# Kernel optimization log

Measured on AMD Instinct MI355X. Metric: run time of the kernel, lower is better.

The kernel has to match this reference:

```python
import jax, jax.numpy as jnp
import numpy as np


def setup_inputs() -> dict:
    key = jax.random.key(0)
    ks = jax.random.split(key, 11)
    B, Cin, H, W = 4, 3, 256, 256
    width, m1, m2, L = 64, 16, 16, 4
    def n(k, shape, scale=1.0):
        return (scale * jax.random.normal(k, shape)).astype(jnp.float32)
    spec_scale = 1.0 / (width * width)  # matches torch scale = 1/(in_ch*out_ch)
    return {
        "x": n(ks[0], (B, Cin, H, W)),
        "fc0_w": n(ks[1], (width, Cin), 0.1),
        "fc0_b": n(ks[2], (width,), 0.1),
        "spec_wr": n(ks[3], (L, width, width, m1, m2), spec_scale),
        "spec_wi": n(ks[4], (L, width, width, m1, m2), spec_scale),
        "w_w": n(ks[5], (L, width, width), 0.1),
        "w_b": n(ks[6], (L, width), 0.1),
        "fc1_w": n(ks[7], (128, width), 0.1),
        "fc1_b": n(ks[8], (128,), 0.1),
        "fc2_w": n(ks[9], (1, 128), 0.1),
        "fc2_b": n(ks[10], (1,), 0.1),
    }


def conv1x1(x, w, b):
    # x: (B,C,H,W), w: (O,C), b: (O,) -- equivalent to nn.Conv2d(C,O,1)
    return jnp.einsum('bchw,oc->bohw', x, w) + b[None, :, None, None]


def spectral_conv2d(x, wr, wi):
    # x: (B,C,H,W); wr/wi: (C,O,m1,m2) real/imag parts of cfloat weight
    B, C, H, W = x.shape
    m1, m2 = wr.shape[2], wr.shape[3]
    O = wr.shape[1]
    x_ft = jnp.fft.rfft2(x)                       # (B,C,H,W//2+1) complex64
    w = wr + 1j * wi
    blk = jnp.einsum('bixy,ioxy->boxy', x_ft[:, :, :m1, :m2], w)
    out_ft = jnp.zeros((B, O, H, W // 2 + 1), dtype=blk.dtype)
    out_ft = out_ft.at[:, :, :m1, :m2].set(blk)
    return jnp.fft.irfft2(out_ft, s=(H, W))


def reference(x, fc0_w, fc0_b, spec_wr, spec_wi, w_w, w_b, fc1_w, fc1_b, fc2_w, fc2_b):
    h = conv1x1(x, fc0_w, fc0_b)
    n_layers = spec_wr.shape[0]
    for i in range(n_layers):
        h = spectral_conv2d(h, spec_wr[i], spec_wi[i]) + conv1x1(h, w_w[i], w_b[i])
        h = jax.nn.gelu(h, approximate=False)
    h = jax.nn.gelu(conv1x1(h, fc1_w, fc1_b), approximate=False)
    return conv1x1(h, fc2_w, fc2_b)
```

## Files before the change

kernel.cpp:

```cpp
#include <hip/hip_runtime.h>
#include <math.h>

#define HW 65536

typedef __attribute__((ext_vector_type(8))) short short8;
typedef __attribute__((ext_vector_type(4))) float f32x4;

__device__ __forceinline__ unsigned bf16rne(float f) {
  union { float f; unsigned u; } a; a.f = f;
  return (a.u + 0x7fffu + ((a.u >> 16) & 1u)) >> 16;
}
__device__ __forceinline__ float bf16tof(unsigned h) {
  union { unsigned u; float f; } a; a.u = h << 16;
  return a.f;
}
__device__ __forceinline__ float gelu(float v) {
  float ax = fabsf(v) * 0.70710678118654752f;
  float t = 1.0f / fmaf(0.3275911f, ax, 1.0f);
  float p = t * (0.254829592f +
           t * (-0.284496736f +
           t * (1.421413741f +
           t * (-1.453152027f +
           t * 1.061405429f))));
  float e = __expf(-ax * ax);
  float er = copysignf(fmaf(-p, e, 1.0f), v);
  return 0.5f * v * (1.0f + er);
}

__global__ __launch_bounds__(256) void k_tables(float* __restrict__ cosT, float* __restrict__ sinT,
                                                ushort* __restrict__ eah, ushort* __restrict__ eal,
                                                ushort* __restrict__ e2h, ushort* __restrict__ e2l,
                                                const float* __restrict__ ww, const float* __restrict__ w1,
                                                ushort* __restrict__ wh, ushort* __restrict__ wl,
                                                ushort* __restrict__ w1h, ushort* __restrict__ w1l) {
  int idx = blockIdx.x * 256 + threadIdx.x;
  const float w = 0.0245436926061702596f;
  if (idx < 4096) {
    int k = idx >> 8, xx = idx & 255;
    int t = (k * xx) & 255;
    float ang = (float)t * w;
    cosT[idx] = cosf(ang);
    sinT[idx] = sinf(ang);
  } else if (idx < 12288) {
    int e = idx - 4096;
    int j = e >> 8, xx = e & 255;
    int k = j >> 1;
    int t = (k * xx) & 255;
    float ang = (float)t * w;
    float val = (j & 1) ? -sinf(ang) : cosf(ang);
    unsigned hi = bf16rne(val);
    unsigned lo = bf16rne(val - bf16tof(hi));
    eah[j * 256 + xx] = (ushort)hi;
    eal[j * 256 + xx] = (ushort)lo;
    e2h[xx * 32 + j] = (ushort)hi;
    e2l[xx * 32 + j] = (ushort)lo;
  } else if (idx < 28672) {
    int j = idx - 12288;
    float v = ww[j];
    unsigned hi = bf16rne(v);
    wh[j] = (ushort)hi;
    wl[j] = (ushort)bf16rne(v - bf16tof(hi));
  } else {
    int j = idx - 28672;
    float v = w1[j];
    unsigned hi = bf16rne(v);
    w1h[j] = (ushort)hi;
    w1l[j] = (ushort)bf16rne(v - bf16tof(hi));
  }
}

__global__ __launch_bounds__(256) void k_fc0(const float* __restrict__ x, const float* __restrict__ w,
                                             const float* __restrict__ b,
                                             const ushort* __restrict__ eah, const ushort* __restrict__ eal,
                                             ushort* __restrict__ hh, float* __restrict__ A2) {
  int bid = blockIdx.x;
  int bb = bid >> 8, y = bid & 255;
  int tid = threadIdx.x;
  __shared__ float ws[192];
  __shared__ float bs[64];
  __shared__ __align__(16) ushort XsH[256 * 66];
  if (tid < 192) ws[tid] = w[tid];
  if (tid < 64) bs[tid] = b[tid];
  __syncthreads();
  const float* xrow = x + ((size_t)(bb * 3) * 256 + y) * 256;
#pragma unroll
  for (int rep = 0; rep < 8; ++rep) {
    int flat = rep * 256 + tid;
    int p = flat >> 3, q = flat & 7;
    float v0 = xrow[p], v1 = xrow[p + HW], v2 = xrow[p + 2 * HW];
    short8 H;
#pragma unroll
    for (int i = 0; i < 8; ++i) {
      int o = q * 8 + i;
      float v = bs[o] + ws[o * 3] * v0 + ws[o * 3 + 1] * v1 + ws[o * 3 + 2] * v2;
      H[i] = (short)bf16rne(v);
    }
    size_t nb = ((size_t)bid * 256 + p) * 64 + q * 8;
    *(short8*)&hh[nb] = H;
    *(short8*)&XsH[p * 66 + q * 8] = H;
  }
  __syncthreads();
  int lane = tid & 63, wv = tid >> 6;
  int lm = lane & 15, lg = lane >> 4;
#pragma unroll
  for (int ntile = 0; ntile < 4; ++ntile) {
    f32x4 dacc[2];
    dacc[0] = (f32x4){0.f, 0.f, 0.f, 0.f};
    dacc[1] = (f32x4){0.f, 0.f, 0.f, 0.f};
#pragma unroll
    for (int kstep = 0; kstep < 2; ++kstep) {
      int x0 = wv * 64 + kstep * 32 + lg * 8;
      short8 bh;
#pragma unroll
      for (int i = 0; i < 8; ++i) {
        bh[i] = (short)XsH[(x0 + i) * 66 + ntile * 16 + lm];
      }
#pragma unroll
      for (int mtile = 0; mtile < 2; ++mtile) {
        short8 ah = *(const short8*)&eah[(mtile * 16 + lm) * 256 + x0];
        short8 al = *(const short8*)&eal[(mtile * 16 + lm) * 256 + x0];
        dacc[mtile] = __builtin_amdgcn_mfma_f32_16x16x32_bf16(ah, bh, dacc[mtile], 0, 0, 0);
        dacc[mtile] = __builtin_amdgcn_mfma_f32_16x16x32_bf16(al, bh, dacc[mtile], 0, 0, 0);
      }
    }
    int c = ntile * 16 + lm;
    size_t row = ((size_t)(bb * 64 + c) * 256 + y) * 128 + wv * 32 + lg * 8;
    *(float4*)&A2[row] = make_float4(dacc[0][0], dacc[0][1], dacc[0][2], dacc[0][3]);
    *(float4*)&A2[row + 4] = make_float4(dacc[1][0], dacc[1][1], dacc[1][2], dacc[1][3]);
  }
}

__global__ __launch_bounds__(256) void k_f2(const float* __restrict__ A2, const float* __restrict__ cosT,
                                            const float* __restrict__ sinT, float2* __restrict__ Xp) {
  int bid = blockIdx.x;
  int plane = bid >> 1, yh = bid & 1;
  int tid = threadIdx.x;
  __shared__ float2 As[128 * 16];
  __shared__ float ct[16 * 129];
  __shared__ float stt[16 * 129];
  const float* Ap = A2 + (size_t)plane * 256 * 128;
#pragma unroll
  for (int rep = 0; rep < 8; ++rep) {
    int flat = rep * 256 + tid;
    int yp = flat >> 4, j = flat & 15;
    int y = yh * 128 + yp;
    int twoj = 2 * j;
    int s = ((twoj >> 2) & 3) * 8 + (twoj >> 4) * 4 + (twoj & 3);
    float2 v = make_float2(0.f, 0.f);
#pragma unroll
    for (int q = 0; q < 4; ++q) {
      float2 a = *(const float2*)&Ap[y * 128 + q * 32 + s];
      v.x += a.x; v.y += a.y;
    }
    As[yp * 16 + j] = v;
  }
#pragma unroll
  for (int rep = 0; rep < 8; ++rep) {
    int flat = rep * 256 + tid;
    int ky = flat >> 7, yp = flat & 127;
    ct[ky * 129 + yp] = cosT[ky * 256 + yh * 128 + yp];
    stt[ky * 129 + yp] = sinT[ky * 256 + yh * 128 + yp];
  }
  __syncthreads();
  int ky = tid >> 4, kx = tid & 15;
  float xr = 0.f, xi = 0.f;
#pragma unroll 4
  for (int yp = 0; yp < 128; ++yp) {
    float2 a = As[yp * 16 + kx];
    float c = ct[ky * 129 + yp], s = stt[ky * 129 + yp];
    xr += c * a.x + s * a.y;
    xi += c * a.y - s * a.x;
  }
  Xp[(size_t)plane * 512 + yh * 256 + tid] = make_float2(xr, xi);
}

__global__ __launch_bounds__(256) void k_mix(const float2* __restrict__ Xp, const float* __restrict__ wr,
                                             const float* __restrict__ wi, float2* __restrict__ Y) {
  int o = blockIdx.x >> 2;
  int mc = blockIdx.x & 3;
  int tid = threadIdx.x;
  int cg = tid >> 6, m2 = tid & 63;
  int m = mc * 64 + m2;
  float yr[4] = {0.f, 0.f, 0.f, 0.f}, yi[4] = {0.f, 0.f, 0.f, 0.f};
#pragma unroll 4
  for (int cc = 0; cc < 16; ++cc) {
    int c = cg * 16 + cc;
    float r = wr[(c * 64 + o) * 256 + m];
    float im = wi[(c * 64 + o) * 256 + m];
#pragma unroll
    for (int b = 0; b < 4; ++b) {
      size_t pb = (size_t)(b * 64 + c) * 512;
      float2 x0 = Xp[pb + m];
      float2 x1 = Xp[pb + 256 + m];
      float xvx = x0.x + x1.x, xvy = x0.y + x1.y;
      yr[b] += xvx * r - xvy * im;
      yi[b] += xvx * im + xvy * r;
    }
  }
  __shared__ float2 red[1024];
#pragma unroll
  for (int b = 0; b < 4; ++b) red[cg * 256 + b * 64 + m2] = make_float2(yr[b], yi[b]);
  __syncthreads();
  int b = tid >> 6;
  float sx = 0.f, sy = 0.f;
#pragma unroll
  for (int g2 = 0; g2 < 4; ++g2) {
    float2 v = red[g2 * 256 + b * 64 + m2];
    sx += v.x; sy += v.y;
  }
  Y[(b * 64 + o) * 256 + m] = make_float2(sx, sy);
}

__global__ __launch_bounds__(256) void k_inv1(const float2* __restrict__ Y, const float* __restrict__ cosT,
                                              const float* __restrict__ sinT,
                                              ushort* __restrict__ gh, ushort* __restrict__ gl) {
  int plane = blockIdx.x;
  int y = threadIdx.x;
  __shared__ float2 Ys[256];
  Ys[threadIdx.x] = Y[plane * 256 + threadIdx.x];
  __syncthreads();
  float gr[16], gi[16];
#pragma unroll
  for (int k = 0; k < 16; ++k) { gr[k] = 0.f; gi[k] = 0.f; }
  for (int ky = 0; ky < 16; ++ky) {
    float c = cosT[ky * 256 + y], s = sinT[ky * 256 + y];
#pragma unroll
    for (int kx = 0; kx < 16; ++kx) {
      float2 v = Ys[ky * 16 + kx];
      gr[kx] += c * v.x - s * v.y;
      gi[kx] += c * v.y + s * v.x;
    }
  }
  float val[32];
  const float sc = 1.0f / 65536.0f;
#pragma unroll
  for (int kx = 0; kx < 16; ++kx) {
    float m = (kx == 0) ? sc : 2.0f * sc;
    val[2 * kx] = gr[kx] * m;
    val[2 * kx + 1] = gi[kx] * m;
  }
  size_t gb = ((size_t)plane * 256 + y) * 32;
#pragma unroll
  for (int q = 0; q < 8; ++q) {
    ushort4 H, L;
#pragma unroll
    for (int r = 0; r < 4; ++r) {
      float v = val[q * 4 + r];
      unsigned hi = bf16rne(v);
      ((ushort*)&H)[r] = (ushort)hi;
      ((ushort*)&L)[r] = (ushort)bf16rne(v - bf16tof(hi));
    }
    *(ushort4*)&gh[gb + q * 4] = H;
    *(ushort4*)&gl[gb + q * 4] = L;
  }
}

__global__ __launch_bounds__(256) void k_layer(const ushort* __restrict__ hh,
                                               const ushort* __restrict__ gh, const ushort* __restrict__ gl,
                                               const ushort* __restrict__ wh, const ushort* __restrict__ wl,
                                               const float* __restrict__ wb,
                                               const ushort* __restrict__ e2h, const ushort* __restrict__ e2l,
                                               const ushort* __restrict__ eah, const ushort* __restrict__ eal,
                                               ushort* __restrict__ oh,
                                               float* __restrict__ A2, int do_dft) {
  int bid = blockIdx.x;
  int b = bid >> 10, y = (bid >> 2) & 255, xq = bid & 3;
  int tid = threadIdx.x;
  int lane = tid & 63, wave = tid >> 6;
  int lm = lane & 15, lg = lane >> 4;
  int x = xq * 64 + wave * 16 + lm;
  size_t nb = (size_t)(b * 256 + y) * 256 + x;

  __shared__ __align__(16) ushort wsH[64 * 72], wsL[64 * 72];
  __shared__ float wbs[64];

#pragma unroll
  for (int rep = 0; rep < 2; ++rep) {
    int flat = rep * 2048 + tid * 8;
    int o = flat >> 6, cc = flat & 63;
    *(short8*)&wsH[o * 72 + cc] = *(const short8*)&wh[flat];
    *(short8*)&wsL[o * 72 + cc] = *(const short8*)&wl[flat];
  }
  if (tid < 64) wbs[tid] = wb[tid];
  __syncthreads();

  short8 bh0 = *(const short8*)&hh[nb * 64 + lg * 8];
  short8 bh1 = *(const short8*)&hh[nb * 64 + 32 + lg * 8];
  short8 eh = *(const short8*)&e2h[x * 32 + lg * 8];
  short8 el = *(const short8*)&e2l[x * 32 + lg * 8];

  f32x4 acc[4];
#pragma unroll
  for (int mi = 0; mi < 4; ++mi) acc[mi] = (f32x4){0.f, 0.f, 0.f, 0.f};

#pragma unroll
  for (int mi = 0; mi < 4; ++mi) {
    int o = mi * 16 + lm;
    short8 ah0 = *(const short8*)&wsH[o * 72 + lg * 8];
    short8 al0 = *(const short8*)&wsL[o * 72 + lg * 8];
    acc[mi] = __builtin_amdgcn_mfma_f32_16x16x32_bf16(ah0, bh0, acc[mi], 0, 0, 0);
    acc[mi] = __builtin_amdgcn_mfma_f32_16x16x32_bf16(al0, bh0, acc[mi], 0, 0, 0);
    short8 ah1 = *(const short8*)&wsH[o * 72 + 32 + lg * 8];
    short8 al1 = *(const short8*)&wsL[o * 72 + 32 + lg * 8];
    acc[mi] = __builtin_amdgcn_mfma_f32_16x16x32_bf16(ah1, bh1, acc[mi], 0, 0, 0);
    acc[mi] = __builtin_amdgcn_mfma_f32_16x16x32_bf16(al1, bh1, acc[mi], 0, 0, 0);
    size_t ga = ((size_t)(b * 64 + o) * 256 + y) * 32 + lg * 8;
    short8 gah = *(const short8*)&gh[ga];
    short8 gal = *(const short8*)&gl[ga];
    acc[mi] = __builtin_amdgcn_mfma_f32_16x16x32_bf16(gah, eh, acc[mi], 0, 0, 0);
    acc[mi] = __builtin_amdgcn_mfma_f32_16x16x32_bf16(gah, el, acc[mi], 0, 0, 0);
    acc[mi] = __builtin_amdgcn_mfma_f32_16x16x32_bf16(gal, eh, acc[mi], 0, 0, 0);
  }

  __syncthreads();
  int xl = wave * 16 + lm;
#pragma unroll
  for (int mi = 0; mi < 4; ++mi) {
    ushort4 H;
#pragma unroll
    for (int r = 0; r < 4; ++r) {
      int o = mi * 16 + lg * 4 + r;
      float ge = gelu(acc[mi][r] + wbs[o]);
      ((ushort*)&H)[r] = (ushort)bf16rne(ge);
    }
    *(ushort4*)&wsH[xl * 66 + mi * 16 + lg * 4] = H;
  }
  __syncthreads();
  size_t rowbase = (size_t)(b * 256 + y) * 256 + xq * 64;
#pragma unroll
  for (int rep = 0; rep < 2; ++rep) {
    int ch = rep * 256 + tid;
    int p = ch >> 3, off = (ch & 7) * 8;
    short8 vH = *(const short8*)&wsH[p * 66 + off];
    *(short8*)&oh[(rowbase + p) * 64 + off] = vH;
  }

  if (do_dft) {
    f32x4 dacc[2];
    dacc[0] = (f32x4){0.f, 0.f, 0.f, 0.f};
    dacc[1] = (f32x4){0.f, 0.f, 0.f, 0.f};
#pragma unroll
    for (int kstep = 0; kstep < 2; ++kstep) {
      int xls = kstep * 32 + lg * 8;
      short8 bh;
#pragma unroll
      for (int i = 0; i < 8; ++i) {
        bh[i] = (short)wsH[(xls + i) * 66 + wave * 16 + lm];
      }
      int x0g = xq * 64 + xls;
#pragma unroll
      for (int mtile = 0; mtile < 2; ++mtile) {
        short8 ah = *(const short8*)&eah[(mtile * 16 + lm) * 256 + x0g];
        short8 al = *(const short8*)&eal[(mtile * 16 + lm) * 256 + x0g];
        dacc[mtile] = __builtin_amdgcn_mfma_f32_16x16x32_bf16(ah, bh, dacc[mtile], 0, 0, 0);
        dacc[mtile] = __builtin_amdgcn_mfma_f32_16x16x32_bf16(al, bh, dacc[mtile], 0, 0, 0);
      }
    }
    int c = wave * 16 + lm;
    size_t row = ((size_t)(b * 64 + c) * 256 + y) * 128 + xq * 32 + lg * 8;
    *(float4*)&A2[row] = make_float4(dacc[0][0], dacc[0][1], dacc[0][2], dacc[0][3]);
    *(float4*)&A2[row + 4] = make_float4(dacc[1][0], dacc[1][1], dacc[1][2], dacc[1][3]);
  }
}

__global__ __launch_bounds__(256) void k_final(const ushort* __restrict__ hh,
                                               const ushort* __restrict__ w1h, const ushort* __restrict__ w1l,
                                               const float* __restrict__ b1, const float* __restrict__ w2,
                                               const float* __restrict__ b2, float* __restrict__ out) {
  int bid = blockIdx.x;
  int b = bid >> 10, y = (bid >> 2) & 255, xq = bid & 3;
  int tid = threadIdx.x;
  int lane = tid & 63, wave = tid >> 6;
  int lm = lane & 15, lg = lane >> 4;
  int x = xq * 64 + wave * 16 + lm;
  size_t nb = (size_t)(b * 256 + y) * 256 + x;

  __shared__ __align__(16) ushort w1sH[128 * 72], w1sL[128 * 72];
  __shared__ float b1s[128], w2s[128];

#pragma unroll
  for (int rep = 0; rep < 4; ++rep) {
    int flat = rep * 2048 + tid * 8;
    int j = flat >> 6, cc = flat & 63;
    *(short8*)&w1sH[j * 72 + cc] = *(const short8*)&w1h[flat];
    *(short8*)&w1sL[j * 72 + cc] = *(const short8*)&w1l[flat];
  }
  if (tid < 128) { b1s[tid] = b1[tid]; w2s[tid] = w2[tid]; }
  __syncthreads();

  short8 bh0 = *(const short8*)&hh[nb * 64 + lg * 8];
  short8 bh1 = *(const short8*)&hh[nb * 64 + 32 + lg * 8];

  f32x4 acc[8];
#pragma unroll
  for (int mi = 0; mi < 8; ++mi) acc[mi] = (f32x4){0.f, 0.f, 0.f, 0.f};

#pragma unroll
  for (int mi = 0; mi < 8; ++mi) {
    int j = mi * 16 + lm;
    short8 ah0 = *(const short8*)&w1sH[j * 72 + lg * 8];
    short8 al0 = *(const short8*)&w1sL[j * 72 + lg * 8];
    acc[mi] = __builtin_amdgcn_mfma_f32_16x16x32_bf16(ah0, bh0, acc[mi], 0, 0, 0);
    acc[mi] = __builtin_amdgcn_mfma_f32_16x16x32_bf16(al0, bh0, acc[mi], 0, 0, 0);
    short8 ah1 = *(const short8*)&w1sH[j * 72 + 32 + lg * 8];
    short8 al1 = *(const short8*)&w1sL[j * 72 + 32 + lg * 8];
    acc[mi] = __builtin_amdgcn_mfma_f32_16x16x32_bf16(ah1, bh1, acc[mi], 0, 0, 0);
    acc[mi] = __builtin_amdgcn_mfma_f32_16x16x32_bf16(al1, bh1, acc[mi], 0, 0, 0);
  }

  float p = 0.f;
#pragma unroll
  for (int mi = 0; mi < 8; ++mi)
#pragma unroll
    for (int r = 0; r < 4; ++r) {
      int j = mi * 16 + lg * 4 + r;
      p += w2s[j] * gelu(acc[mi][r] + b1s[j]);
    }
  p += __shfl_xor(p, 16);
  p += __shfl_xor(p, 32);
  if (lg == 0) {
    out[(b * 256 + y) * 256 + x] = p + b2[0];
  }
}

extern "C" void kernel_launch(void* const* d_in, const int* in_sizes, int n_in,
                              void* d_out, int out_size, void* d_ws, size_t ws_size,
                              hipStream_t stream) {
  const float* x       = (const float*)d_in[0];
  const float* fc0_w   = (const float*)d_in[1];
  const float* fc0_b   = (const float*)d_in[2];
  const float* spec_wr = (const float*)d_in[3];
  const float* spec_wi = (const float*)d_in[4];
  const float* w_w     = (const float*)d_in[5];
  const float* w_b     = (const float*)d_in[6];
  const float* fc1_w   = (const float*)d_in[7];
  const float* fc1_b   = (const float*)d_in[8];
  const float* fc2_w   = (const float*)d_in[9];
  const float* fc2_b   = (const float*)d_in[10];
  float* out = (float*)d_out;

  char* ws = (char*)d_ws;
  ushort* h0h  = (ushort*)ws;
  ushort* h1h  = (ushort*)(ws + 33554432);
  float*  A2   = (float*)(ws + 67108864);
  ushort* gh   = (ushort*)(ws + 100663296);
  ushort* gl   = (ushort*)(ws + 104857600);
  float2* Xp   = (float2*)(ws + 109051904);
  float2* Y    = (float2*)(ws + 110100480);
  float*  cosT = (float*)(ws + 110624768);
  float*  sinT = (float*)(ws + 110641152);
  ushort* eah  = (ushort*)(ws + 110657536);
  ushort* eal  = (ushort*)(ws + 110673920);
  ushort* e2h  = (ushort*)(ws + 110690304);
  ushort* e2l  = (ushort*)(ws + 110706688);
  ushort* wWh  = (ushort*)(ws + 110723072);
  ushort* wWl  = (ushort*)(ws + 110755840);
  ushort* w1h  = (ushort*)(ws + 110788608);
  ushort* w1l  = (ushort*)(ws + 110804992);

  k_tables<<<144, 256, 0, stream>>>(cosT, sinT, eah, eal, e2h, e2l,
                                    w_w, fc1_w, wWh, wWl, w1h, w1l);
  k_fc0<<<1024, 256, 0, stream>>>(x, fc0_w, fc0_b, eah, eal, h0h, A2);
  ushort* hch = h0h;
  ushort* hnh = h1h;
  for (int l = 0; l < 4; ++l) {
    k_f2<<<512, 256, 0, stream>>>(A2, cosT, sinT, Xp);
    k_mix<<<256, 256, 0, stream>>>(Xp, spec_wr + (size_t)l * 1048576, spec_wi + (size_t)l * 1048576, Y);
    k_inv1<<<256, 256, 0, stream>>>(Y, cosT, sinT, gh, gl);
    k_layer<<<4096, 256, 0, stream>>>(hch, gh, gl, wWh + l * 4096, wWl + l * 4096,
                                      w_b + l * 64, e2h, e2l, eah, eal, hnh, A2, (l < 3) ? 1 : 0);
    ushort* t = hch; hch = hnh; hnh = t;
  }
  k_final<<<4096, 256, 0, stream>>>(hch, w1h, w1l, fc1_b, fc2_w, fc2_b, out);
}
```

Baseline: 367.5 us.

## Process full image rows per block in k_layer and compute full x-DFT in-block

k_layer now handles a whole 256-pixel row per block (1024 blocks instead of 4096). Each wave computes a 4x4 grid of MFMA tiles, and the spectral g-tile is staged in shared memory and reused across the row. Because the row-wise DFT along x now covers the full row inside one block, the partial-sum buffer shrinks from four quarter-row partials to one, and k_f2 no longer has to sum them. The intended savings are fewer partial writes and reads, less redundant weight and g loading, and less per-block overhead, at the cost of more registers (a 16-tile accumulator) and fewer blocks to fill the device.

New measurement: 342.3 us. -6.8%, faster.

```diff
diff --git a/kernel.cpp b/kernel.cpp
--- a/kernel.cpp
+++ b/kernel.cpp
@@ -72,7 +72,7 @@
 __global__ __launch_bounds__(256) void k_fc0(const float* __restrict__ x, const float* __restrict__ w,
                                              const float* __restrict__ b,
                                              const ushort* __restrict__ eah, const ushort* __restrict__ eal,
-                                             ushort* __restrict__ hh, float* __restrict__ A2) {
+                                             ushort* __restrict__ hh, float* __restrict__ A) {
   int bid = blockIdx.x;
   int bb = bid >> 8, y = bid & 255;
   int tid = threadIdx.x;
@@ -102,35 +102,30 @@
   __syncthreads();
   int lane = tid & 63, wv = tid >> 6;
   int lm = lane & 15, lg = lane >> 4;
-#pragma unroll
-  for (int ntile = 0; ntile < 4; ++ntile) {
-    f32x4 dacc[2];
-    dacc[0] = (f32x4){0.f, 0.f, 0.f, 0.f};
-    dacc[1] = (f32x4){0.f, 0.f, 0.f, 0.f};
-#pragma unroll
-    for (int kstep = 0; kstep < 2; ++kstep) {
-      int x0 = wv * 64 + kstep * 32 + lg * 8;
-      short8 bh;
-#pragma unroll
-      for (int i = 0; i < 8; ++i) {
-        bh[i] = (short)XsH[(x0 + i) * 66 + ntile * 16 + lm];
-      }
-#pragma unroll
-      for (int mtile = 0; mtile < 2; ++mtile) {
-        short8 ah = *(const short8*)&eah[(mtile * 16 + lm) * 256 + x0];
-        short8 al = *(const short8*)&eal[(mtile * 16 + lm) * 256 + x0];
-        dacc[mtile] = __builtin_amdgcn_mfma_f32_16x16x32_bf16(ah, bh, dacc[mtile], 0, 0, 0);
-        dacc[mtile] = __builtin_amdgcn_mfma_f32_16x16x32_bf16(al, bh, dacc[mtile], 0, 0, 0);
-      }
-    }
-    int c = ntile * 16 + lm;
-    size_t row = ((size_t)(bb * 64 + c) * 256 + y) * 128 + wv * 32 + lg * 8;
-    *(float4*)&A2[row] = make_float4(dacc[0][0], dacc[0][1], dacc[0][2], dacc[0][3]);
-    *(float4*)&A2[row + 4] = make_float4(dacc[1][0], dacc[1][1], dacc[1][2], dacc[1][3]);
-  }
-}
-
-__global__ __launch_bounds__(256) void k_f2(const float* __restrict__ A2, const float* __restrict__ cosT,
+  f32x4 d0 = (f32x4){0.f, 0.f, 0.f, 0.f};
+  f32x4 d1 = (f32x4){0.f, 0.f, 0.f, 0.f};
+  int c = wv * 16 + lm;
+#pragma unroll
+  for (int kc = 0; kc < 8; ++kc) {
+    int x0 = kc * 32 + lg * 8;
+    short8 bh;
+#pragma unroll
+    for (int i = 0; i < 8; ++i) bh[i] = (short)XsH[(x0 + i) * 66 + c];
+    short8 a0h = *(const short8*)&eah[lm * 256 + x0];
+    short8 a0l = *(const short8*)&eal[lm * 256 + x0];
+    short8 a1h = *(const short8*)&eah[(16 + lm) * 256 + x0];
+    short8 a1l = *(const short8*)&eal[(16 + lm) * 256 + x0];
+    d0 = __builtin_amdgcn_mfma_f32_16x16x32_bf16(a0h, bh, d0, 0, 0, 0);
+    d0 = __builtin_amdgcn_mfma_f32_16x16x32_bf16(a0l, bh, d0, 0, 0, 0);
+    d1 = __builtin_amdgcn_mfma_f32_16x16x32_bf16(a1h, bh, d1, 0, 0, 0);
+    d1 = __builtin_amdgcn_mfma_f32_16x16x32_bf16(a1l, bh, d1, 0, 0, 0);
+  }
+  size_t row = ((size_t)(bb * 64 + c) * 256 + y) * 32;
+  *(float4*)&A[row + lg * 4] = make_float4(d0[0], d0[1], d0[2], d0[3]);
+  *(float4*)&A[row + 16 + lg * 4] = make_float4(d1[0], d1[1], d1[2], d1[3]);
+}
+
+__global__ __launch_bounds__(256) void k_f2(const float* __restrict__ A, const float* __restrict__ cosT,
                                             const float* __restrict__ sinT, float2* __restrict__ Xp) {
   int bid = blockIdx.x;
   int plane = bid >> 1, yh = bid & 1;
@@ -138,21 +133,11 @@
   __shared__ float2 As[128 * 16];
   __shared__ float ct[16 * 129];
   __shared__ float stt[16 * 129];
-  const float* Ap = A2 + (size_t)plane * 256 * 128;
+  const float2* Ap = (const float2*)A + (size_t)plane * 4096;
 #pragma unroll
   for (int rep = 0; rep < 8; ++rep) {
     int flat = rep * 256 + tid;
-    int yp = flat >> 4, j = flat & 15;
-    int y = yh * 128 + yp;
-    int twoj = 2 * j;
-    int s = ((twoj >> 2) & 3) * 8 + (twoj >> 4) * 4 + (twoj & 3);
-    float2 v = make_float2(0.f, 0.f);
-#pragma unroll
-    for (int q = 0; q < 4; ++q) {
-      float2 a = *(const float2*)&Ap[y * 128 + q * 32 + s];
-      v.x += a.x; v.y += a.y;
-    }
-    As[yp * 16 + j] = v;
+    As[flat] = Ap[yh * 2048 + flat];
   }
 #pragma unroll
   for (int rep = 0; rep < 8; ++rep) {
@@ -262,17 +247,21 @@
                                                const ushort* __restrict__ e2h, const ushort* __restrict__ e2l,
                                                const ushort* __restrict__ eah, const ushort* __restrict__ eal,
                                                ushort* __restrict__ oh,
-                                               float* __restrict__ A2, int do_dft) {
+                                               float* __restrict__ A, int do_dft) {
   int bid = blockIdx.x;
-  int b = bid >> 10, y = (bid >> 2) & 255, xq = bid & 3;
+  int b = bid >> 8, y = bid & 255;
   int tid = threadIdx.x;
-  int lane = tid & 63, wave = tid >> 6;
+  int lane = tid & 63, wv = tid >> 6;
   int lm = lane & 15, lg = lane >> 4;
-  int x = xq * 64 + wave * 16 + lm;
-  size_t nb = (size_t)(b * 256 + y) * 256 + x;
-
-  __shared__ __align__(16) ushort wsH[64 * 72], wsL[64 * 72];
+  size_t nbase = (size_t)(b * 256 + y) * 256;
+
+  __shared__ __align__(16) ushort smem[16896];
   __shared__ float wbs[64];
+  ushort* wsH = smem;
+  ushort* wsL = smem + 4608;
+  ushort* gsH = smem + 9216;
+  ushort* gsL = smem + 11776;
+  ushort* Xs  = smem;
 
 #pragma unroll
   for (int rep = 0; rep < 2; ++rep) {
@@ -281,85 +270,99 @@
     *(short8*)&wsH[o * 72 + cc] = *(const short8*)&wh[flat];
     *(short8*)&wsL[o * 72 + cc] = *(const short8*)&wl[flat];
   }
+  {
+    int o = tid >> 2, i = (tid & 3) * 8;
+    size_t ga = ((size_t)(b * 64 + o) * 256 + y) * 32 + i;
+    *(short8*)&gsH[o * 40 + i] = *(const short8*)&gh[ga];
+    *(short8*)&gsL[o * 40 + i] = *(const short8*)&gl[ga];
+  }
   if (tid < 64) wbs[tid] = wb[tid];
   __syncthreads();
 
-  short8 bh0 = *(const short8*)&hh[nb * 64 + lg * 8];
-  short8 bh1 = *(const short8*)&hh[nb * 64 + 32 + lg * 8];
-  short8 eh = *(const short8*)&e2h[x * 32 + lg * 8];
-  short8 el = *(const short8*)&e2l[x * 32 + lg * 8];
-
-  f32x4 acc[4];
-#pragma unroll
-  for (int mi = 0; mi < 4; ++mi) acc[mi] = (f32x4){0.f, 0.f, 0.f, 0.f};
+  short8 bh0[4], bh1[4], ehv[4], elv[4];
+#pragma unroll
+  for (int ni = 0; ni < 4; ++ni) {
+    int xx = wv * 64 + ni * 16 + lm;
+    size_t hb = (nbase + xx) * 64 + lg * 8;
+    bh0[ni] = *(const short8*)&hh[hb];
+    bh1[ni] = *(const short8*)&hh[hb + 32];
+    ehv[ni] = *(const short8*)&e2h[xx * 32 + lg * 8];
+    elv[ni] = *(const short8*)&e2l[xx * 32 + lg * 8];
+  }
+
+  f32x4 acc[4][4];
+#pragma unroll
+  for (int mi = 0; mi < 4; ++mi)
+#pragma unroll
+    for (int ni = 0; ni < 4; ++ni) acc[mi][ni] = (f32x4){0.f, 0.f, 0.f, 0.f};
 
 #pragma unroll
   for (int mi = 0; mi < 4; ++mi) {
     int o = mi * 16 + lm;
     short8 ah0 = *(const short8*)&wsH[o * 72 + lg * 8];
     short8 al0 = *(const short8*)&wsL[o * 72 + lg * 8];
-    acc[mi] = __builtin_amdgcn_mfma_f32_16x16x32_bf16(ah0, bh0, acc[mi], 0, 0, 0);
-    acc[mi] = __builtin_amdgcn_mfma_f32_16x16x32_bf16(al0, bh0, acc[mi], 0, 0, 0);
     short8 ah1 = *(const short8*)&wsH[o * 72 + 32 + lg * 8];
     short8 al1 = *(const short8*)&wsL[o * 72 + 32 + lg * 8];
-    acc[mi] = __builtin_amdgcn_mfma_f32_16x16x32_bf16(ah1, bh1, acc[mi], 0, 0, 0);
-    acc[mi] = __builtin_amdgcn_mfma_f32_16x16x32_bf16(al1, bh1, acc[mi], 0, 0, 0);
-    size_t ga = ((size_t)(b * 64 + o) * 256 + y) * 32 + lg * 8;
-    short8 gah = *(const short8*)&gh[ga];
-    short8 gal = *(const short8*)&gl[ga];
-    acc[mi] = __builtin_amdgcn_mfma_f32_16x16x32_bf16(gah, eh, acc[mi], 0, 0, 0);
-    acc[mi] = __builtin_amdgcn_mfma_f32_16x16x32_bf16(gah, el, acc[mi], 0, 0, 0);
-    acc[mi] = __builtin_amdgcn_mfma_f32_16x16x32_bf16(gal, eh, acc[mi], 0, 0, 0);
-  }
-
-  __syncthreads();
-  int xl = wave * 16 + lm;
-#pragma unroll
-  for (int mi = 0; mi < 4; ++mi) {
-    ushort4 H;
-#pragma unroll
-    for (int r = 0; r < 4; ++r) {
-      int o = mi * 16 + lg * 4 + r;
-      float ge = gelu(acc[mi][r] + wbs[o]);
-      ((ushort*)&H)[r] = (ushort)bf16rne(ge);
-    }
-    *(ushort4*)&wsH[xl * 66 + mi * 16 + lg * 4] = H;
-  }
-  __syncthreads();
-  size_t rowbase = (size_t)(b * 256 + y) * 256 + xq * 64;
-#pragma unroll
-  for (int rep = 0; rep < 2; ++rep) {
-    int ch = rep * 256 + tid;
-    int p = ch >> 3, off = (ch & 7) * 8;
-    short8 vH = *(const short8*)&wsH[p * 66 + off];
-    *(short8*)&oh[(rowbase + p) * 64 + off] = vH;
+    short8 gah = *(const short8*)&gsH[o * 40 + lg * 8];
+    short8 gal = *(const short8*)&gsL[o * 40 + lg * 8];
+#pragma unroll
+    for (int ni = 0; ni < 4; ++ni) {
+      acc[mi][ni] = __builtin_amdgcn_mfma_f32_16x16x32_bf16(ah0, bh0[ni], acc[mi][ni], 0, 0, 0);
+      acc[mi][ni] = __builtin_amdgcn_mfma_f32_16x16x32_bf16(al0, bh0[ni], acc[mi][ni], 0, 0, 0);
+      acc[mi][ni] = __builtin_amdgcn_mfma_f32_16x16x32_bf16(ah1, bh1[ni], acc[mi][ni], 0, 0, 0);
+      acc[mi][ni] = __builtin_amdgcn_mfma_f32_16x16x32_bf16(al1, bh1[ni], acc[mi][ni], 0, 0, 0);
+      acc[mi][ni] = __builtin_amdgcn_mfma_f32_16x16x32_bf16(gah, ehv[ni], acc[mi][ni], 0, 0, 0);
+      acc[mi][ni] = __builtin_amdgcn_mfma_f32_16x16x32_bf16(gah, elv[ni], acc[mi][ni], 0, 0, 0);
+      acc[mi][ni] = __builtin_amdgcn_mfma_f32_16x16x32_bf16(gal, ehv[ni], acc[mi][ni], 0, 0, 0);
+    }
+  }
+
+  __syncthreads();
+#pragma unroll
+  for (int mi = 0; mi < 4; ++mi)
+#pragma unroll
+    for (int ni = 0; ni < 4; ++ni) {
+      int xx = wv * 64 + ni * 16 + lm;
+      ushort4 H;
+#pragma unroll
+      for (int r = 0; r < 4; ++r) {
+        int o = mi * 16 + lg * 4 + r;
+        float ge = gelu(acc[mi][ni][r] + wbs[o]);
+        ((ushort*)&H)[r] = (ushort)bf16rne(ge);
+      }
+      *(ushort4*)&Xs[xx * 66 + mi * 16 + lg * 4] = H;
+    }
+  __syncthreads();
+#pragma unroll
+  for (int rep = 0; rep < 8; ++rep) {
+    int flat = rep * 256 + tid;
+    int p = flat >> 3, off = (flat & 7) * 8;
+    short8 vH = *(const short8*)&Xs[p * 66 + off];
+    *(short8*)&oh[(nbase + p) * 64 + off] = vH;
   }
 
   if (do_dft) {
-    f32x4 dacc[2];
-    dacc[0] = (f32x4){0.f, 0.f, 0.f, 0.f};
-    dacc[1] = (f32x4){0.f, 0.f, 0.f, 0.f};
-#pragma unroll
-    for (int kstep = 0; kstep < 2; ++kstep) {
-      int xls = kstep * 32 + lg * 8;
+    f32x4 d0 = (f32x4){0.f, 0.f, 0.f, 0.f};
+    f32x4 d1 = (f32x4){0.f, 0.f, 0.f, 0.f};
+    int c = wv * 16 + lm;
+#pragma unroll
+    for (int kc = 0; kc < 8; ++kc) {
+      int x0 = kc * 32 + lg * 8;
       short8 bh;
 #pragma unroll
-      for (int i = 0; i < 8; ++i) {
-        bh[i] = (short)wsH[(xls + i) * 66 + wave * 16 + lm];
-      }
-      int x0g = xq * 64 + xls;
-#pragma unroll
-      for (int mtile = 0; mtile < 2; ++mtile) {
-        short8 ah = *(const short8*)&eah[(mtile * 16 + lm) * 256 + x0g];
-        short8 al = *(const short8*)&eal[(mtile * 16 + lm) * 256 + x0g];
-        dacc[mtile] = __builtin_amdgcn_mfma_f32_16x16x32_bf16(ah, bh, dacc[mtile], 0, 0, 0);
-        dacc[mtile] = __builtin_amdgcn_mfma_f32_16x16x32_bf16(al, bh, dacc[mtile], 0, 0, 0);
-      }
-    }
-    int c = wave * 16 + lm;
-    size_t row = ((size_t)(b * 64 + c) * 256 + y) * 128 + xq * 32 + lg * 8;
-    *(float4*)&A2[row] = make_float4(dacc[0][0], dacc[0][1], dacc[0][2], dacc[0][3]);
-    *(float4*)&A2[row + 4] = make_float4(dacc[1][0], dacc[1][1], dacc[1][2], dacc[1][3]);
+      for (int i = 0; i < 8; ++i) bh[i] = (short)Xs[(x0 + i) * 66 + c];
+      short8 a0h = *(const short8*)&eah[lm * 256 + x0];
+      short8 a0l = *(const short8*)&eal[lm * 256 + x0];
+      short8 a1h = *(const short8*)&eah[(16 + lm) * 256 + x0];
+      short8 a1l = *(const short8*)&eal[(16 + lm) * 256 + x0];
+      d0 = __builtin_amdgcn_mfma_f32_16x16x32_bf16(a0h, bh, d0, 0, 0, 0);
+      d0 = __builtin_amdgcn_mfma_f32_16x16x32_bf16(a0l, bh, d0, 0, 0, 0);
+      d1 = __builtin_amdgcn_mfma_f32_16x16x32_bf16(a1h, bh, d1, 0, 0, 0);
+      d1 = __builtin_amdgcn_mfma_f32_16x16x32_bf16(a1l, bh, d1, 0, 0, 0);
+    }
+    size_t row = ((size_t)(b * 64 + c) * 256 + y) * 32;
+    *(float4*)&A[row + lg * 4] = make_float4(d0[0], d0[1], d0[2], d0[3]);
+    *(float4*)&A[row + 16 + lg * 4] = make_float4(d1[0], d1[1], d1[2], d1[3]);
   }
 }
 
@@ -442,33 +445,33 @@
   char* ws = (char*)d_ws;
   ushort* h0h  = (ushort*)ws;
   ushort* h1h  = (ushort*)(ws + 33554432);
-  float*  A2   = (float*)(ws + 67108864);
-  ushort* gh   = (ushort*)(ws + 100663296);
-  ushort* gl   = (ushort*)(ws + 104857600);
-  float2* Xp   = (float2*)(ws + 109051904);
-  float2* Y    = (float2*)(ws + 110100480);
-  float*  cosT = (float*)(ws + 110624768);
-  float*  sinT = (float*)(ws + 110641152);
-  ushort* eah  = (ushort*)(ws + 110657536);
-  ushort* eal  = (ushort*)(ws + 110673920);
-  ushort* e2h  = (ushort*)(ws + 110690304);
-  ushort* e2l  = (ushort*)(ws + 110706688);
-  ushort* wWh  = (ushort*)(ws + 110723072);
-  ushort* wWl  = (ushort*)(ws + 110755840);
-  ushort* w1h  = (ushort*)(ws + 110788608);
-  ushort* w1l  = (ushort*)(ws + 110804992);
+  float*  A    = (float*)(ws + 67108864);
+  ushort* gh   = (ushort*)(ws + 75497472);
+  ushort* gl   = (ushort*)(ws + 79691776);
+  float2* Xp   = (float2*)(ws + 83886080);
+  float2* Y    = (float2*)(ws + 84934656);
+  float*  cosT = (float*)(ws + 85458944);
+  float*  sinT = (float*)(ws + 85475328);
+  ushort* eah  = (ushort*)(ws + 85491712);
+  ushort* eal  = (ushort*)(ws + 85508096);
+  ushort* e2h  = (ushort*)(ws + 85524480);
+  ushort* e2l  = (ushort*)(ws + 85540864);
+  ushort* wWh  = (ushort*)(ws + 85557248);
+  ushort* wWl  = (ushort*)(ws + 85590016);
+  ushort* w1h  = (ushort*)(ws + 85622784);
+  ushort* w1l  = (ushort*)(ws + 85639168);
 
   k_tables<<<144, 256, 0, stream>>>(cosT, sinT, eah, eal, e2h, e2l,
                                     w_w, fc1_w, wWh, wWl, w1h, w1l);
-  k_fc0<<<1024, 256, 0, stream>>>(x, fc0_w, fc0_b, eah, eal, h0h, A2);
+  k_fc0<<<1024, 256, 0, stream>>>(x, fc0_w, fc0_b, eah, eal, h0h, A);
   ushort* hch = h0h;
   ushort* hnh = h1h;
   for (int l = 0; l < 4; ++l) {
-    k_f2<<<512, 256, 0, stream>>>(A2, cosT, sinT, Xp);
+    k_f2<<<512, 256, 0, stream>>>(A, cosT, sinT, Xp);
     k_mix<<<256, 256, 0, stream>>>(Xp, spec_wr + (size_t)l * 1048576, spec_wi + (size_t)l * 1048576, Y);
     k_inv1<<<256, 256, 0, stream>>>(Y, cosT, sinT, gh, gl);
-    k_layer<<<4096, 256, 0, stream>>>(hch, gh, gl, wWh + l * 4096, wWl + l * 4096,
-                                      w_b + l * 64, e2h, e2l, eah, eal, hnh, A2, (l < 3) ? 1 : 0);
+    k_layer<<<1024, 256, 0, stream>>>(hch, gh, gl, wWh + l * 4096, wWl + l * 4096,
+                                      w_b + l * 64, e2h, e2l, eah, eal, hnh, A, (l < 3) ? 1 : 0);
     ushort* t = hch; hch = hnh; hnh = t;
   }
   k_final<<<4096, 256, 0, stream>>>(hch, w1h, w1l, fc1_b, fc2_w, fc2_b, out);
```
